# Kernel optimization log

Hardware: AMD Instinct MI355X
Metric: run time of the kernel (lower is better)

## Reference

```python
import jax, jax.numpy as jnp
import numpy as np

L, D, H, KV, HD, FF, V = 2, 2048, 16, 8, 128, 6144, 32000
B, T = 1, 2048
THETA = 1.0e6
EPS = 1e-6
NEG = -1e30


def _rope_tables():
    inv = 1.0 / (THETA ** (np.arange(0, HD, 2, dtype=np.float32) / HD))
    ang = np.arange(T, dtype=np.float32)[:, None] * inv[None, :]
    ang = np.concatenate([ang, ang], axis=1)  # [T, HD]
    return jnp.asarray(np.cos(ang), jnp.float32), jnp.asarray(np.sin(ang), jnp.float32)


def _rmsnorm(x, scale):
    v = jnp.mean(x * x, axis=-1, keepdims=True)
    return x * jax.lax.rsqrt(v + EPS) * scale


def _rope(x, cos, sin):
    # x: [B, h, T, HD]; rotate-half RoPE with full-dim cos/sin tables
    x1, x2 = x[..., : HD // 2], x[..., HD // 2 :]
    rot = jnp.concatenate([-x2, x1], axis=-1)
    return x * cos[None, None] + rot * sin[None, None]


def setup_inputs() -> dict:
    key = jax.random.key(0)
    ks = jax.random.split(key, 12)
    s = 0.02
    return {
        "token_ids": jax.random.randint(ks[0], (B, T), 0, V),
        "emb": jax.random.normal(ks[1], (V, D), jnp.float32) * s,
        "Wq": jax.random.normal(ks[2], (L, D, H * HD), jnp.float32) * s,
        "Wk": jax.random.normal(ks[3], (L, D, KV * HD), jnp.float32) * s,
        "Wv": jax.random.normal(ks[4], (L, D, KV * HD), jnp.float32) * s,
        "Wo": jax.random.normal(ks[5], (L, H * HD, D), jnp.float32) * s,
        "qn": jnp.ones((L, HD), jnp.float32),
        "kn": jnp.ones((L, HD), jnp.float32),
        "W1": jax.random.normal(ks[6], (L, D, FF), jnp.float32) * s,
        "W2": jax.random.normal(ks[7], (L, D, FF), jnp.float32) * s,
        "W3": jax.random.normal(ks[8], (L, FF, D), jnp.float32) * s,
        "ln1": jnp.ones((L, D), jnp.float32),
        "ln2": jnp.ones((L, D), jnp.float32),
        "lnf": jnp.ones((D,), jnp.float32),
    }


def reference(token_ids, emb, Wq, Wk, Wv, Wo, qn, kn, W1, W2, W3, ln1, ln2, lnf):
    cos, sin = _rope_tables()
    x = emb[token_ids]  # [B, T, D]
    causal = jnp.tril(jnp.ones((T, T), dtype=bool))
    G = H // KV
    scale = 1.0 / np.sqrt(HD)
    for l in range(L):
        # attention block
        h = _rmsnorm(x, ln1[l])
        q = (h @ Wq[l]).reshape(B, T, H, HD).transpose(0, 2, 1, 3)   # [B,H,T,HD]
        k = (h @ Wk[l]).reshape(B, T, KV, HD).transpose(0, 2, 1, 3)  # [B,KV,T,HD]
        v = (h @ Wv[l]).reshape(B, T, KV, HD).transpose(0, 2, 1, 3)
        q = _rmsnorm(q, qn[l])
        k = _rmsnorm(k, kn[l])
        q = _rope(q, cos, sin)
        k = _rope(k, cos, sin)
        qg = q.reshape(B, KV, G, T, HD)
        s_att = jnp.einsum("bgqtd,bgsd->bgqts", qg, k) * scale
        s_att = jnp.where(causal, s_att, NEG)
        a = jax.nn.softmax(s_att, axis=-1)
        o = jnp.einsum("bgqts,bgsd->bgqtd", a, v)
        o = o.reshape(B, H, T, HD).transpose(0, 2, 1, 3).reshape(B, T, H * HD)
        x = x + o @ Wo[l]
        # SwiGLU FFN block
        h = _rmsnorm(x, ln2[l])
        x = x + (jax.nn.silu(h @ W1[l]) * (h @ W2[l])) @ W3[l]
    x = _rmsnorm(x, lnf)
    return x @ emb.T  # tied lm head -> [B, T, V]
```

## Files before the change

kernel.cpp:

```cpp
#include <hip/hip_runtime.h>
#include <math.h>

typedef float f32x4 __attribute__((ext_vector_type(4)));
typedef __bf16 bf16x8 __attribute__((ext_vector_type(8)));
typedef unsigned short u16x8 __attribute__((ext_vector_type(8)));

static constexpr int Dm  = 2048;
static constexpr int Tm  = 2048;
static constexpr int Hm  = 16;
static constexpr int KVm = 8;
static constexpr int HDm = 128;
static constexpr int FFm = 6144;
static constexpr int Vm  = 32000;
static constexpr int QKVN = 4096;

__device__ __forceinline__ float b2f(unsigned short u) {
  unsigned int x = ((unsigned int)u) << 16;
  return __builtin_bit_cast(float, x);
}
__device__ __forceinline__ unsigned short f2b(float f) {
  return __builtin_bit_cast(unsigned short, (__bf16)f);
}
__device__ __forceinline__ f32x4 mfma16x16x32(bf16x8 a, bf16x8 b, f32x4 c) {
  return __builtin_amdgcn_mfma_f32_16x16x32_bf16(a, b, c, 0, 0, 0);
}

__device__ __forceinline__ void gload16(const void* g, void* lds) {
  __builtin_amdgcn_global_load_lds(
      (const __attribute__((address_space(1))) unsigned int*)g,
      (__attribute__((address_space(3))) unsigned int*)lds, 16, 0, 0);
}

__device__ __forceinline__ int xcd_swz(int o, int nwg) {
  int q = nwg >> 3, r8 = nwg & 7;
  int xcd = o & 7, pos = o >> 3;
  return (xcd < r8) ? xcd * (q + 1) + pos : r8 * (q + 1) + (xcd - r8) * q + pos;
}

__global__ void rope_tables_k(float* __restrict__ cosT, float* __restrict__ sinT) {
  int t = blockIdx.x;
  int i = threadIdx.x;
  double inv = pow(1000000.0, -(double)i / 64.0);
  double ang = (double)t * inv;
  cosT[t * 64 + i] = (float)cos(ang);
  sinT[t * 64 + i] = (float)sin(ang);
}

__global__ __launch_bounds__(256) void embed_k(const int* __restrict__ ids,
                                               const float* __restrict__ emb,
                                               float* __restrict__ x) {
  int t = blockIdx.x;
  int d0 = threadIdx.x * 8;
  int id = ids[t];
  const float* src = emb + (size_t)id * Dm + d0;
  float* dst = x + (size_t)t * Dm + d0;
  *(f32x4*)dst       = *(const f32x4*)src;
  *(f32x4*)(dst + 4) = *(const f32x4*)(src + 4);
}

__global__ __launch_bounds__(256) void rmsnorm_k(const float* __restrict__ x,
                                                 const float* __restrict__ g,
                                                 unsigned short* __restrict__ y) {
  int t = blockIdx.x;
  const float* xr = x + (size_t)t * Dm;
  float vals[8];
  float s = 0.f;
#pragma unroll
  for (int i = 0; i < 8; ++i) {
    float vv = xr[threadIdx.x + i * 256];
    vals[i] = vv;
    s += vv * vv;
  }
#pragma unroll
  for (int off = 32; off; off >>= 1) s += __shfl_xor(s, off);
  __shared__ float red[4];
  if ((threadIdx.x & 63) == 0) red[threadIdx.x >> 6] = s;
  __syncthreads();
  s = (red[0] + red[1]) + (red[2] + red[3]);
  float r = rsqrtf(s * (1.f / Dm) + 1e-6f);
  unsigned short* yr = y + (size_t)t * Dm;
#pragma unroll
  for (int i = 0; i < 8; ++i) {
    int d = threadIdx.x + i * 256;
    yr[d] = f2b(vals[i] * r * g[d]);
  }
}

__global__ __launch_bounds__(256) void qknorm_rope_k(unsigned short* __restrict__ q,
                                                     const float* __restrict__ nrm,
                                                     const float* __restrict__ cosT,
                                                     const float* __restrict__ sinT,
                                                     int nheads) {
  int gw = (int)((blockIdx.x * blockDim.x + threadIdx.x) >> 6);
  int lane = threadIdx.x & 63;
  int t = gw / nheads, h = gw % nheads;
  unsigned short* row = q + ((size_t)t * nheads + h) * HDm;
  float x1 = b2f(row[lane]);
  float x2 = b2f(row[lane + 64]);
  float s = x1 * x1 + x2 * x2;
#pragma unroll
  for (int off = 32; off; off >>= 1) s += __shfl_xor(s, off);
  float r = rsqrtf(s * (1.f / HDm) + 1e-6f);
  float y1 = x1 * r * nrm[lane];
  float y2 = x2 * r * nrm[lane + 64];
  float c = cosT[t * 64 + lane];
  float sn = sinT[t * 64 + lane];
  row[lane]      = f2b(y1 * c - y2 * sn);
  row[lane + 64] = f2b(y2 * c + y1 * sn);
}

__global__ __launch_bounds__(256) void cvtT_k(const float* __restrict__ W,
                                              unsigned short* __restrict__ Wt,
                                              int K, int N) {
  __shared__ __align__(16) unsigned short tile[64][68];
  const int n0 = blockIdx.x * 64, k0 = blockIdx.y * 64;
  const int tid = threadIdx.x;
#pragma unroll
  for (int i = 0; i < 4; ++i) {
    int e = tid + i * 256;
    int r = e >> 4, c4 = (e & 15) * 4;
    f32x4 v = *(const f32x4*)(W + (size_t)(k0 + r) * N + n0 + c4);
    tile[r][c4 + 0] = f2b(v.x);
    tile[r][c4 + 1] = f2b(v.y);
    tile[r][c4 + 2] = f2b(v.z);
    tile[r][c4 + 3] = f2b(v.w);
  }
  __syncthreads();
#pragma unroll
  for (int i = 0; i < 2; ++i) {
    int e = tid + i * 256;
    int rr = e >> 3, cc = (e & 7) * 8;
    u16x8 o;
#pragma unroll
    for (int j = 0; j < 8; ++j) o[j] = tile[cc + j][rr];
    *(u16x8*)(Wt + (size_t)(n0 + rr) * K + k0 + cc) = o;
  }
}

template <int EPI, bool BF32, bool OUTF32>
__global__ __launch_bounds__(256) void gemm_k(const unsigned short* __restrict__ A,
                                              const void* __restrict__ B,
                                              void* __restrict__ C,
                                              void* __restrict__ C2,
                                              void* __restrict__ C3,
                                              int N, int K, int cOff) {
  __shared__ __align__(16) unsigned short As[128 * 32];
  __shared__ __align__(16) unsigned short Bs[128 * 32];
  const int tid = threadIdx.x;
  const int nwg = gridDim.x * gridDim.y;
  const int nid = xcd_swz(blockIdx.x + gridDim.x * blockIdx.y, nwg);
  const int bm = nid % gridDim.x, bn = nid / gridDim.x;
  const int w = tid >> 6, lane = tid & 63;
  const int wm = (w >> 1) * 64, wn = (w & 1) * 64;
  const int lr = lane & 15, hi = lane >> 4, kq = hi * 8;
  const int rowA0 = bm * 128, colB0 = bn * 128;

  const int sr = lane >> 2;
  const int sc = (lane & 3) * 8;
  const unsigned short* a0 = A + (size_t)(rowA0 + (w * 2 + 0) * 16 + sr) * K + sc;
  const unsigned short* a1 = A + (size_t)(rowA0 + (w * 2 + 1) * 16 + sr) * K + sc;
  unsigned short* la0 = &As[(w * 2 + 0) * 512];
  unsigned short* la1 = &As[(w * 2 + 1) * 512];
  const unsigned short* b0 = nullptr; const unsigned short* b1 = nullptr;
  unsigned short* lb0 = &Bs[(w * 2 + 0) * 512];
  unsigned short* lb1 = &Bs[(w * 2 + 1) * 512];
  if (!BF32) {
    b0 = (const unsigned short*)B + (size_t)(colB0 + (w * 2 + 0) * 16 + sr) * K + sc;
    b1 = (const unsigned short*)B + (size_t)(colB0 + (w * 2 + 1) * 16 + sr) * K + sc;
  }

  f32x4 acc[4][4] = {};

  for (int k0 = 0; k0 < K; k0 += 32) {
    __syncthreads();
    gload16(a0 + k0, la0);
    gload16(a1 + k0, la1);
    if (!BF32) {
      gload16(b0 + k0, lb0);
      gload16(b1 + k0, lb1);
    } else {
#pragma unroll
      for (int i = 0; i < 2; ++i) {
        int e = tid + i * 256;
        int rr = e >> 2, cc = (e & 3) * 8;
        const float* bp = (const float*)B + (size_t)(colB0 + rr) * K + k0 + cc;
        f32x4 v0 = *(const f32x4*)bp;
        f32x4 v1 = *(const f32x4*)(bp + 4);
        u16x8 o;
        o[0] = f2b(v0.x); o[1] = f2b(v0.y); o[2] = f2b(v0.z); o[3] = f2b(v0.w);
        o[4] = f2b(v1.x); o[5] = f2b(v1.y); o[6] = f2b(v1.z); o[7] = f2b(v1.w);
        *(u16x8*)&Bs[rr * 32 + cc] = o;
      }
    }
    __syncthreads();

    bf16x8 av[4], bv[4];
#pragma unroll
    for (int m = 0; m < 4; ++m)
      av[m] = __builtin_bit_cast(bf16x8, *(const u16x8*)&As[(wm + m * 16 + lr) * 32 + kq]);
#pragma unroll
    for (int n = 0; n < 4; ++n)
      bv[n] = __builtin_bit_cast(bf16x8, *(const u16x8*)&Bs[(wn + n * 16 + lr) * 32 + kq]);
#pragma unroll
    for (int m = 0; m < 4; ++m)
#pragma unroll
      for (int n = 0; n < 4; ++n)
        acc[m][n] = mfma16x16x32(av[m], bv[n], acc[m][n]);
  }

  const int r0 = rowA0 + wm + hi * 4;
  const int c0 = wn + lr;
#pragma unroll
  for (int m = 0; m < 4; ++m)
#pragma unroll
    for (int n = 0; n < 4; ++n) {
      const int cc = colB0 + c0 + n * 16;
#pragma unroll
      for (int j = 0; j < 4; ++j) {
        int r = r0 + m * 16 + j;
        if (EPI == 0) {
          size_t idx = (size_t)r * N + cOff + cc;
          if (OUTF32) ((float*)C)[idx] = acc[m][n][j];
          else        ((unsigned short*)C)[idx] = f2b(acc[m][n][j]);
        } else if (EPI == 1) {
          ((float*)C)[(size_t)r * N + cc] += acc[m][n][j];
        } else if (EPI == 2) {
          unsigned short* Cb = (unsigned short*)C;
          size_t idx = (size_t)r * N + cc;
          float gg = b2f(Cb[idx]);
          gg = gg / (1.f + __expf(-gg));
          Cb[idx] = f2b(gg * acc[m][n][j]);
        } else {
          unsigned short v = f2b(acc[m][n][j]);
          if (cc < 2048)      ((unsigned short*)C )[(size_t)r * 2048 + cc] = v;
          else if (cc < 3072) ((unsigned short*)C2)[(size_t)r * 1024 + (cc - 2048)] = v;
          else                ((unsigned short*)C3)[(size_t)r * 1024 + (cc - 3072)] = v;
        }
      }
    }
}

__global__ __launch_bounds__(256) void attn_k(const unsigned short* __restrict__ qg,
                                              const unsigned short* __restrict__ kg,
                                              const unsigned short* __restrict__ vg,
                                              unsigned short* __restrict__ og) {
  __shared__ __align__(16) unsigned short Ks[64 * 128];
  __shared__ __align__(16) unsigned short Vt[128 * 72];
  __shared__ __align__(16) unsigned short Pl[4 * 16 * 72];
  const int tid = threadIdx.x;
  const int nid = xcd_swz(blockIdx.x + (blockIdx.y << 4), 256);
  const int pr = nid & 15, h = nid >> 4;
  const int w = tid >> 6, lane = tid & 63;
  const int lr = lane & 15, hi = lane >> 4;
  const int kvh = h >> 1;

  size_t goff[4]; unsigned kdst[4]; int vr[4], vc[4];
#pragma unroll
  for (int i = 0; i < 4; ++i) {
    int e = tid + i * 256;
    int r = e >> 4, c = (e & 15) * 8;
    goff[i] = ((size_t)r * KVm + kvh) * HDm + c;
    kdst[i] = (unsigned)((r * 256 + c * 2) ^ ((r & 7) << 4));
    vr[i] = r; vc[i] = c;
  }

  for (int pass = 0; pass < 2; ++pass) {
    const int qt = pass ? (31 - pr) : pr;
    const int t0 = qt * 64;
    const int ntk = qt + 1;

    bf16x8 qa[4];
    {
      const unsigned short* qrow = qg + ((size_t)(t0 + w * 16 + lr) * Hm + h) * HDm;
#pragma unroll
      for (int ks = 0; ks < 4; ++ks)
        qa[ks] = __builtin_bit_cast(bf16x8, *(const u16x8*)(qrow + ks * 32 + hi * 8));
    }

    f32x4 oa[8] = {};
    float mj[4], lj[4];
#pragma unroll
    for (int j = 0; j < 4; ++j) { mj[j] = -3.0e38f; lj[j] = 0.f; }

    u16x8 kk[4], vv[4];
#pragma unroll
    for (int i = 0; i < 4; ++i) {
      kk[i] = *(const u16x8*)(kg + goff[i]);
      vv[i] = *(const u16x8*)(vg + goff[i]);
    }

    for (int t = 0; t < ntk; ++t) {
      __syncthreads();
#pragma unroll
      for (int i = 0; i < 4; ++i) {
        *(u16x8*)((char*)Ks + kdst[i]) = kk[i];
#pragma unroll
        for (int j = 0; j < 8; ++j) {
          int d = vc[i] + j;
          Vt[d * 72 + (vr[i] ^ (((d >> 3) & 7) << 3))] = vv[i][j];
        }
      }
      if (t + 1 < ntk) {
        size_t add = (size_t)(t + 1) * 64 * KVm * HDm;
#pragma unroll
        for (int i = 0; i < 4; ++i) {
          kk[i] = *(const u16x8*)(kg + goff[i] + add);
          vv[i] = *(const u16x8*)(vg + goff[i] + add);
        }
      }
      __syncthreads();

      const int s0 = t * 64;
      f32x4 s[4] = {};
#pragma unroll
      for (int ks = 0; ks < 4; ++ks)
#pragma unroll
        for (int nt = 0; nt < 4; ++nt) {
          int krow = nt * 16 + lr;
          int kbyte = (krow * 256 + (ks * 32 + hi * 8) * 2) ^ ((krow & 7) << 4);
          bf16x8 kf = __builtin_bit_cast(bf16x8, *(const u16x8*)((char*)Ks + kbyte));
          s[nt] = mfma16x16x32(qa[ks], kf, s[nt]);
        }

      float p[4][4];
      const bool maskt = (t == ntk - 1);
#pragma unroll
      for (int nt = 0; nt < 4; ++nt)
#pragma unroll
        for (int j = 0; j < 4; ++j) {
          float val = s[nt][j] * 0.08838834764831845f;
          if (maskt && (s0 + nt * 16 + lr) > (t0 + w * 16 + hi * 4 + j)) val = -1e30f;
          p[nt][j] = val;
        }

#pragma unroll
      for (int j = 0; j < 4; ++j) {
        float mx = fmaxf(fmaxf(p[0][j], p[1][j]), fmaxf(p[2][j], p[3][j]));
#pragma unroll
        for (int msk = 1; msk < 16; msk <<= 1) mx = fmaxf(mx, __shfl_xor(mx, msk));
        float mnew = fmaxf(mj[j], mx);
        float alpha = __expf(mj[j] - mnew);
        mj[j] = mnew;
        float sum = 0.f;
#pragma unroll
        for (int nt = 0; nt < 4; ++nt) {
          float e = __expf(p[nt][j] - mnew);
          p[nt][j] = e;
          sum += e;
        }
#pragma unroll
        for (int msk = 1; msk < 16; msk <<= 1) sum += __shfl_xor(sum, msk);
        lj[j] = lj[j] * alpha + sum;
#pragma unroll
        for (int nt2 = 0; nt2 < 8; ++nt2) oa[nt2][j] *= alpha;
      }

#pragma unroll
      for (int nt = 0; nt < 4; ++nt)
#pragma unroll
        for (int j = 0; j < 4; ++j)
          Pl[(w * 16 + hi * 4 + j) * 72 + nt * 16 + lr] = f2b(p[nt][j]);
      __builtin_amdgcn_sched_barrier(0);

      bf16x8 pa[2];
#pragma unroll
      for (int ks2 = 0; ks2 < 2; ++ks2)
        pa[ks2] = __builtin_bit_cast(bf16x8,
                   *(const u16x8*)&Pl[(w * 16 + lr) * 72 + ks2 * 32 + hi * 8]);
#pragma unroll
      for (int nt2 = 0; nt2 < 8; ++nt2)
#pragma unroll
        for (int ks2 = 0; ks2 < 2; ++ks2) {
          int d = nt2 * 16 + lr;
          int kv = ks2 * 32 + hi * 8;
          bf16x8 vf = __builtin_bit_cast(bf16x8,
                       *(const u16x8*)&Vt[d * 72 + (kv ^ (((d >> 3) & 7) << 3))]);
          oa[nt2] = mfma16x16x32(pa[ks2], vf, oa[nt2]);
        }
    }

#pragma unroll
    for (int nt2 = 0; nt2 < 8; ++nt2)
#pragma unroll
      for (int j = 0; j < 4; ++j) {
        int row = t0 + w * 16 + hi * 4 + j;
        int d = nt2 * 16 + lr;
        og[((size_t)row * Hm + h) * HDm + d] = f2b(oa[nt2][j] / lj[j]);
      }
  }
}

extern "C" void kernel_launch(void* const* d_in, const int* in_sizes, int n_in,
                              void* d_out, int out_size, void* d_ws, size_t ws_size,
                              hipStream_t stream) {
  (void)in_sizes; (void)n_in; (void)out_size; (void)ws_size;
  const int*   ids = (const int*)d_in[0];
  const float* emb = (const float*)d_in[1];
  const float* Wq  = (const float*)d_in[2];
  const float* Wk  = (const float*)d_in[3];
  const float* Wv  = (const float*)d_in[4];
  const float* Wo  = (const float*)d_in[5];
  const float* qn  = (const float*)d_in[6];
  const float* kn  = (const float*)d_in[7];
  const float* W1  = (const float*)d_in[8];
  const float* W2  = (const float*)d_in[9];
  const float* W3  = (const float*)d_in[10];
  const float* ln1 = (const float*)d_in[11];
  const float* ln2 = (const float*)d_in[12];
  const float* lnf = (const float*)d_in[13];

  char* p = (char*)d_ws;
  float* xf          = (float*)p;          p += (size_t)Tm * Dm * 4;
  unsigned short* hb = (unsigned short*)p; p += (size_t)Tm * Dm * 2;
  float* cosT        = (float*)p;          p += (size_t)Tm * 64 * 4;
  float* sinT        = (float*)p;          p += (size_t)Tm * 64 * 4;
  unsigned short* qb = (unsigned short*)p; p += (size_t)Tm * Hm * HDm * 2;
  unsigned short* kb = (unsigned short*)p; p += (size_t)Tm * KVm * HDm * 2;
  unsigned short* vb = (unsigned short*)p; p += (size_t)Tm * KVm * HDm * 2;
  unsigned short* ob = (unsigned short*)p; p += (size_t)Tm * Hm * HDm * 2;
  unsigned short* wt = (unsigned short*)p; p += (size_t)Dm * FFm * 2;
  unsigned short* g1 = qb;

  rope_tables_k<<<Tm, 64, 0, stream>>>(cosT, sinT);
  embed_k<<<Tm, 256, 0, stream>>>(ids, emb, xf);

  for (int l = 0; l < 2; ++l) {
    const float* Wq_l = Wq + (size_t)l * Dm * (Hm * HDm);
    const float* Wk_l = Wk + (size_t)l * Dm * (KVm * HDm);
    const float* Wv_l = Wv + (size_t)l * Dm * (KVm * HDm);
    const float* Wo_l = Wo + (size_t)l * (Hm * HDm) * Dm;
    const float* W1_l = W1 + (size_t)l * Dm * FFm;
    const float* W2_l = W2 + (size_t)l * Dm * FFm;
    const float* W3_l = W3 + (size_t)l * FFm * Dm;

    rmsnorm_k<<<Tm, 256, 0, stream>>>(xf, ln1 + (size_t)l * Dm, hb);

    cvtT_k<<<dim3((Hm * HDm) / 64, Dm / 64), 256, 0, stream>>>(Wq_l, wt, Dm, Hm * HDm);
    cvtT_k<<<dim3((KVm * HDm) / 64, Dm / 64), 256, 0, stream>>>(
        Wk_l, wt + (size_t)2048 * Dm, Dm, KVm * HDm);
    cvtT_k<<<dim3((KVm * HDm) / 64, Dm / 64), 256, 0, stream>>>(
        Wv_l, wt + (size_t)3072 * Dm, Dm, KVm * HDm);
    gemm_k<3, false, false><<<dim3(Tm / 128, QKVN / 128), 256, 0, stream>>>(
        hb, wt, qb, kb, vb, QKVN, Dm, 0);

    qknorm_rope_k<<<(Tm * Hm) / 4, 256, 0, stream>>>(qb, qn + (size_t)l * HDm, cosT, sinT, Hm);
    qknorm_rope_k<<<(Tm * KVm) / 4, 256, 0, stream>>>(kb, kn + (size_t)l * HDm, cosT, sinT, KVm);

    attn_k<<<dim3(16, 16), 256, 0, stream>>>(qb, kb, vb, ob);

    cvtT_k<<<dim3(Dm / 64, (Hm * HDm) / 64), 256, 0, stream>>>(Wo_l, wt, Hm * HDm, Dm);
    gemm_k<1, false, false><<<dim3(Tm / 128, Dm / 128), 256, 0, stream>>>(
        ob, wt, xf, nullptr, nullptr, Dm, Hm * HDm, 0);

    rmsnorm_k<<<Tm, 256, 0, stream>>>(xf, ln2 + (size_t)l * Dm, hb);

    cvtT_k<<<dim3(FFm / 64, Dm / 64), 256, 0, stream>>>(W1_l, wt, Dm, FFm);
    gemm_k<0, false, false><<<dim3(Tm / 128, FFm / 128), 256, 0, stream>>>(
        hb, wt, g1, nullptr, nullptr, FFm, Dm, 0);
    cvtT_k<<<dim3(FFm / 64, Dm / 64), 256, 0, stream>>>(W2_l, wt, Dm, FFm);
    gemm_k<2, false, false><<<dim3(Tm / 128, FFm / 128), 256, 0, stream>>>(
        hb, wt, g1, nullptr, nullptr, FFm, Dm, 0);
    cvtT_k<<<dim3(Dm / 64, FFm / 64), 256, 0, stream>>>(W3_l, wt, FFm, Dm);
    gemm_k<1, false, false><<<dim3(Tm / 128, Dm / 128), 256, 0, stream>>>(
        g1, wt, xf, nullptr, nullptr, Dm, FFm, 0);
  }

  rmsnorm_k<<<Tm, 256, 0, stream>>>(xf, lnf, hb);

  gemm_k<0, true, true><<<dim3(Tm / 128, Vm / 128), 256, 0, stream>>>(
      hb, emb, d_out, nullptr, nullptr, Vm, Dm, 0);
}
```

Baseline: 1.639 ms.

## Add 256x256 8-wave GEMM kernel for FFN up/gate and chunked LM head

Adds a new 256x256-tile GEMM with 512 threads, double-buffered LDS, a four-phase interleaved load/MMA schedule and setprio hints, and uses it for the W1 and W2 FFN projections. The LM head now first converts the fp32 embedding table to bf16 in chunks, reusing the qb buffer as scratch, and runs the new GEMM on each chunk instead of the old kernel that read fp32 B directly. This aims for higher arithmetic intensity and cheaper B loads, at the cost of extra conversion kernels. The 256-wide tiles also give fewer workgroups, which may leave some CUs idle.

```diff
diff --git a/kernel.cpp b/kernel.cpp
--- a/kernel.cpp
+++ b/kernel.cpp
@@ -56,6 +56,17 @@
   float* dst = x + (size_t)t * Dm + d0;
   *(f32x4*)dst       = *(const f32x4*)src;
   *(f32x4*)(dst + 4) = *(const f32x4*)(src + 4);
+}
+
+__global__ __launch_bounds__(256) void cvt_flat_k(const float* __restrict__ src,
+                                                  unsigned short* __restrict__ dst) {
+  size_t i = ((size_t)blockIdx.x * 256 + threadIdx.x) * 8;
+  f32x4 a = *(const f32x4*)(src + i);
+  f32x4 b = *(const f32x4*)(src + i + 4);
+  u16x8 o;
+  o[0] = f2b(a.x); o[1] = f2b(a.y); o[2] = f2b(a.z); o[3] = f2b(a.w);
+  o[4] = f2b(b.x); o[5] = f2b(b.y); o[6] = f2b(b.z); o[7] = f2b(b.w);
+  *(u16x8*)(dst + i) = o;
 }
 
 __global__ __launch_bounds__(256) void rmsnorm_k(const float* __restrict__ x,
@@ -240,6 +251,126 @@
     }
 }
 
+#define LDA256(MH)                                                             \
+  _Pragma("unroll") for (int m_ = 0; m_ < 4; ++m_)                             \
+  _Pragma("unroll") for (int ks_ = 0; ks_ < 2; ++ks_)                          \
+    av[m_][ks_] = *(const bf16x8*)&Ac[aBase + (MH) * 4096 + m_ * 1024 + uu[ks_]];
+#define LDB256(NH)                                                             \
+  _Pragma("unroll") for (int n_ = 0; n_ < 2; ++n_)                             \
+  _Pragma("unroll") for (int ks_ = 0; ks_ < 2; ++ks_)                          \
+    bv[n_][ks_] = *(const bf16x8*)&Bc[bBase + (NH) * 2048 + n_ * 1024 + uu[ks_]];
+#define MMA256(MH, NH)                                                         \
+  __builtin_amdgcn_s_setprio(1);                                               \
+  _Pragma("unroll") for (int m_ = 0; m_ < 4; ++m_)                             \
+  _Pragma("unroll") for (int n_ = 0; n_ < 2; ++n_)                             \
+  _Pragma("unroll") for (int ks_ = 0; ks_ < 2; ++ks_)                          \
+    acc[(MH) * 4 + m_][(NH) * 2 + n_] = mfma16x16x32(                          \
+        av[m_][ks_], bv[n_][ks_], acc[(MH) * 4 + m_][(NH) * 2 + n_]);          \
+  __builtin_amdgcn_s_setprio(0);
+#define SYNCV                                                                  \
+  asm volatile("s_waitcnt vmcnt(4)" ::: "memory");                             \
+  __builtin_amdgcn_s_barrier();                                                \
+  asm volatile("s_waitcnt lgkmcnt(0)" ::: "memory");                           \
+  __builtin_amdgcn_sched_barrier(0);
+#define SYNCNV                                                                 \
+  __builtin_amdgcn_s_barrier();                                                \
+  asm volatile("s_waitcnt lgkmcnt(0)" ::: "memory");                           \
+  __builtin_amdgcn_sched_barrier(0);
+#define ENDPH __builtin_amdgcn_s_barrier();
+
+template <int EPI, bool OUTF32>
+__global__ __launch_bounds__(512) void gemm256_k(const unsigned short* __restrict__ A,
+                                                 const unsigned short* __restrict__ B,
+                                                 void* __restrict__ C,
+                                                 int N, int K, int cOff) {
+  __shared__ __align__(16) unsigned short lds[2][2][256 * 64];
+  const int tid = threadIdx.x;
+  const int nwg = gridDim.x * gridDim.y;
+  const int nid = xcd_swz(blockIdx.x + gridDim.x * blockIdx.y, nwg);
+  const int bm = nid % gridDim.x, bn = nid / gridDim.x;
+  const int w = tid >> 6, lane = tid & 63;
+  const int wr = w >> 2, wc = w & 3;
+  const int lr = lane & 15, hi = lane >> 4;
+  const int rowA0 = bm * 256, colB0 = bn * 256;
+  const int nk = K >> 6;
+
+  const int srow = lane >> 3;
+  const int ulog = (lane & 7) ^ srow;
+  const int eaR = (w < 4) ? w * 16 : 128 + (w - 4) * 16;
+  const int laR = eaR + 64;
+  const int ebR = (w >> 1) * 64 + (w & 1) * 16;
+  const int lbR = ebR + 32;
+  const unsigned short* gAt = A + (size_t)rowA0 * K + ulog * 8;
+  const unsigned short* gBt = B + (size_t)colB0 * K + ulog * 8;
+
+  int uu[2];
+  uu[0] = ((0 + hi) ^ (lr & 7)) * 8;
+  uu[1] = ((4 + hi) ^ (lr & 7)) * 8;
+  const int aBase = (wr * 128 + lr) * 64;
+  const int bBase = (wc * 64 + lr) * 64;
+
+  f32x4 acc[8][4] = {};
+  bf16x8 av[4][2], bv[2][2];
+
+  auto stage2 = [&](const unsigned short* g, int rbase, unsigned short* l, int k0) {
+    gload16(g + (size_t)(rbase + srow) * K + k0, l + rbase * 64);
+    gload16(g + (size_t)(rbase + 8 + srow) * K + k0, l + (rbase + 8) * 64);
+  };
+
+  stage2(gAt, eaR, &lds[0][0][0], 0);
+  stage2(gBt, ebR, &lds[0][1][0], 0);
+  stage2(gBt, lbR, &lds[0][1][0], 0);
+  stage2(gAt, laR, &lds[0][0][0], 0);
+  asm volatile("s_waitcnt vmcnt(0)" ::: "memory");
+  __builtin_amdgcn_s_barrier();
+
+  for (int kt = 0; kt < nk; ++kt) {
+    unsigned short* Ac = &lds[kt & 1][0][0];
+    unsigned short* Bc = &lds[kt & 1][1][0];
+    unsigned short* An = &lds[(kt + 1) & 1][0][0];
+    unsigned short* Bn = &lds[(kt + 1) & 1][1][0];
+    const int k0n = (kt + 1) << 6;
+    const bool more = (kt + 1) < nk;
+
+    LDA256(0) LDB256(0)
+    if (more) stage2(gAt, eaR, An, k0n);
+    SYNCV MMA256(0, 0) ENDPH
+    LDB256(1)
+    if (more) stage2(gBt, ebR, Bn, k0n);
+    SYNCV MMA256(0, 1) ENDPH
+    LDA256(1)
+    if (more) stage2(gBt, lbR, Bn, k0n);
+    SYNCNV MMA256(1, 1) ENDPH
+    LDB256(0)
+    if (more) stage2(gAt, laR, An, k0n);
+    SYNCV MMA256(1, 0) ENDPH
+  }
+
+  const int r0 = rowA0 + wr * 128 + hi * 4;
+  const int c0 = colB0 + wc * 64 + lr;
+#pragma unroll
+  for (int mi = 0; mi < 8; ++mi)
+#pragma unroll
+    for (int n = 0; n < 4; ++n) {
+      const int cc = c0 + n * 16;
+#pragma unroll
+      for (int j = 0; j < 4; ++j) {
+        int r = r0 + mi * 16 + j;
+        if (EPI == 0) {
+          size_t idx = (size_t)r * N + cOff + cc;
+          if (OUTF32) ((float*)C)[idx] = acc[mi][n][j];
+          else        ((unsigned short*)C)[idx] = f2b(acc[mi][n][j]);
+        } else {
+          unsigned short* Cb = (unsigned short*)C;
+          size_t idx = (size_t)r * N + cc;
+          float gg = b2f(Cb[idx]);
+          gg = gg / (1.f + __expf(-gg));
+          Cb[idx] = f2b(gg * acc[mi][n][j]);
+        }
+      }
+    }
+}
+
 __global__ __launch_bounds__(256) void attn_k(const unsigned short* __restrict__ qg,
                                               const unsigned short* __restrict__ kg,
                                               const unsigned short* __restrict__ vg,
@@ -455,11 +586,11 @@
     rmsnorm_k<<<Tm, 256, 0, stream>>>(xf, ln2 + (size_t)l * Dm, hb);
 
     cvtT_k<<<dim3(FFm / 64, Dm / 64), 256, 0, stream>>>(W1_l, wt, Dm, FFm);
-    gemm_k<0, false, false><<<dim3(Tm / 128, FFm / 128), 256, 0, stream>>>(
-        hb, wt, g1, nullptr, nullptr, FFm, Dm, 0);
+    gemm256_k<0, false><<<dim3(Tm / 256, FFm / 256), 512, 0, stream>>>(
+        hb, wt, g1, FFm, Dm, 0);
     cvtT_k<<<dim3(FFm / 64, Dm / 64), 256, 0, stream>>>(W2_l, wt, Dm, FFm);
-    gemm_k<2, false, false><<<dim3(Tm / 128, FFm / 128), 256, 0, stream>>>(
-        hb, wt, g1, nullptr, nullptr, FFm, Dm, 0);
+    gemm256_k<2, false><<<dim3(Tm / 256, FFm / 256), 512, 0, stream>>>(
+        hb, wt, g1, FFm, Dm, 0);
     cvtT_k<<<dim3(Dm / 64, FFm / 64), 256, 0, stream>>>(W3_l, wt, FFm, Dm);
     gemm_k<1, false, false><<<dim3(Tm / 128, Dm / 128), 256, 0, stream>>>(
         g1, wt, xf, nullptr, nullptr, Dm, FFm, 0);
@@ -467,6 +598,14 @@
 
   rmsnorm_k<<<Tm, 256, 0, stream>>>(xf, lnf, hb);
 
-  gemm_k<0, true, true><<<dim3(Tm / 128, Vm / 128), 256, 0, stream>>>(
-      hb, emb, d_out, nullptr, nullptr, Vm, Dm, 0);
-}
+  unsigned short* embB = qb;
+  const int chunks[3] = {12288, 12288, 7424};
+  int off = 0;
+  for (int c = 0; c < 3; ++c) {
+    const int rows = chunks[c];
+    cvt_flat_k<<<rows, 256, 0, stream>>>(emb + (size_t)off * Dm, embB);
+    gemm256_k<0, true><<<dim3(Tm / 256, rows / 256), 512, 0, stream>>>(
+        hb, embB, d_out, Vm, Dm, off);
+    off += rows;
+  }
+}
```

Result: faster. 1.553 ms (-5.2%).
